# Kernel tuning notes

Hardware: AMD Instinct MI355X
Metric: run time of the kernel (lower is better)

## Reference

```python
import jax, jax.numpy as jnp
import numpy as np

B, C, H, W = 8, 256, 128, 128
CQ = C // 8


def setup_inputs() -> dict:
    key = jax.random.key(0)
    ks = jax.random.split(key, 8)
    s = 1.0 / np.sqrt(C)
    return {
        "x": jax.random.normal(ks[0], (B, C, H, W), dtype=jnp.float32),
        "wq": jax.random.normal(ks[1], (CQ, C), dtype=jnp.float32) * s,
        "bq": jax.random.normal(ks[2], (CQ,), dtype=jnp.float32) * 0.01,
        "wk": jax.random.normal(ks[3], (CQ, C), dtype=jnp.float32) * s,
        "bk": jax.random.normal(ks[4], (CQ,), dtype=jnp.float32) * 0.01,
        "wv": jax.random.normal(ks[5], (C, C), dtype=jnp.float32) * s,
        "bv": jax.random.normal(ks[6], (C,), dtype=jnp.float32) * 0.01,
        "gamma": jax.random.normal(ks[7], (1,), dtype=jnp.float32) * 0.1,
    }


def reference(x, wq, bq, wk, bk, wv, bv, gamma):
    b, c, h, w = x.shape
    # 1x1 convs == channel matmuls
    q = jnp.einsum("oc,bchw->bohw", wq, x) + bq[None, :, None, None]  # [B,Cq,H,W]
    k = jnp.einsum("oc,bchw->bohw", wk, x) + bk[None, :, None, None]  # [B,Cq,H,W]
    v = jnp.einsum("oc,bchw->bohw", wv, x) + bv[None, :, None, None]  # [B,C,H,W]

    # column (height) scores: energy_H[b,i,w,j] = <k[:, i, w], q[:, j, w]>, -inf on i==j
    e_h = jnp.einsum("bciw,bcjw->biwj", k, q)  # [B,H,W,H]
    diag = jnp.eye(h, dtype=bool)[:, None, :]  # [H,1,H] -> masks i==j
    e_h = jnp.where(diag[None], -jnp.inf, e_h)

    # row (width) scores: energy_W[b,h,i,j] = <k[:, h, i], q[:, h, j]>
    e_w = jnp.einsum("bchi,bchj->bhij", k, q)  # [B,H,W,W]

    # joint softmax over concatenated H+W scores (axis 3), as in the torch code
    att = jax.nn.softmax(jnp.concatenate([e_h, e_w], axis=3), axis=3)
    a_h, a_w = att[..., :h], att[..., h:]

    out_h = jnp.einsum("bciw,biwj->bcjw", v, a_h)  # aggregate along column
    out_w = jnp.einsum("bchi,bhij->bchj", v, a_w)  # aggregate along row
    return gamma * (out_h + out_w) + x
```

## Files before the change

### kernel.cpp

```cpp
#include <hip/hip_runtime.h>
#include <math.h>

#define C_   256
#define CQ_  32
#define H_   128
#define W_   128
#define HW_  (H_ * W_)
#define OC_  320

typedef __attribute__((ext_vector_type(8))) short  s8v;
typedef __attribute__((ext_vector_type(4))) float  f4v;
typedef __attribute__((ext_vector_type(8))) unsigned short u8v;
typedef __attribute__((ext_vector_type(4))) unsigned short u4v;

__device__ inline unsigned short f2bf(float f) {
    unsigned int u = __float_as_uint(f);
    unsigned int r = (u + 0x7fffu + ((u >> 16) & 1u)) >> 16;
    return (unsigned short)r;
}
__device__ inline float bfu(unsigned short u) {
    return __uint_as_float((unsigned int)u << 16);
}

__global__ __launch_bounds__(256) void k_wconv(
    const float* __restrict__ wq, const float* __restrict__ wk,
    const float* __restrict__ wv, unsigned short* __restrict__ Wb)
{
    int idx4 = blockIdx.x * 256 + threadIdx.x;
    int e = idx4 * 4;
    int oc = e >> 8, k = e & 255;
    const float* src;
    if (oc < 32)      src = wq + (size_t)oc * C_ + k;
    else if (oc < 64) src = wk + (size_t)(oc - 32) * C_ + k;
    else              src = wv + (size_t)(oc - 64) * C_ + k;
    float4 v = *(const float4*)src;
    u4v o;
    o[0] = f2bf(v.x); o[1] = f2bf(v.y); o[2] = f2bf(v.z); o[3] = f2bf(v.w);
    *(u4v*)(Wb + e) = o;
}

__global__ __launch_bounds__(256) void k_qkv(
    const float* __restrict__ x, const unsigned short* __restrict__ Wb,
    const float* __restrict__ bq, const float* __restrict__ bk,
    const float* __restrict__ bv,
    unsigned short* __restrict__ qkv, int b0)
{
    __shared__ __align__(16) unsigned short Wl[160][72];
    __shared__ __align__(16) unsigned int   Xp[32 * 132];
    const int t = threadIdx.x;
    const int lane = t & 63;
    const int wave = t >> 6;
    const int n0 = blockIdx.x * 128;
    const int ocblk = blockIdx.y * 160;
    const int bb = blockIdx.z;
    const float* xb = x + (size_t)(b0 + bb) * C_ * HW_;

    const int lg = lane >> 4;
    const int ll = lane & 15;
    const int n_w = wave * 32;

    const int kp8 = t >> 5;
    const int n4  = (t & 31) * 4;
    const int wrow = t >> 3;
    const int wcg  = (t & 7) * 8;
    float4 ra[4], rb[4];
    u8v wreg[5];

    #pragma unroll
    for (int p = 0; p < 4; ++p) {
        int krow = (p * 8 + kp8) * 2;
        ra[p] = *(const float4*)(xb + (size_t)krow * HW_ + n0 + n4);
        rb[p] = *(const float4*)(xb + (size_t)(krow + 1) * HW_ + n0 + n4);
    }
    #pragma unroll
    for (int q = 0; q < 5; ++q)
        wreg[q] = *(const u8v*)(Wb + (size_t)(ocblk + wrow + q * 32) * C_ + wcg);

    f4v acc[10][2];
    #pragma unroll
    for (int mr = 0; mr < 10; ++mr)
        #pragma unroll
        for (int nr = 0; nr < 2; ++nr)
            acc[mr][nr] = (f4v){0.f, 0.f, 0.f, 0.f};

    #pragma unroll
    for (int kc = 0; kc < 4; ++kc) {
        __syncthreads();
        #pragma unroll
        for (int p = 0; p < 4; ++p) {
            uint4 d;
            const float* af  = (const float*)&ra[p];
            const float* bf_ = (const float*)&rb[p];
            #pragma unroll
            for (int i = 0; i < 4; ++i) {
                unsigned int lo = (__float_as_uint(af[i])  + 0x8000u) >> 16;
                unsigned int hi = (__float_as_uint(bf_[i]) + 0x8000u) & 0xffff0000u;
                ((unsigned int*)&d)[i] = hi | lo;
            }
            *(uint4*)&Xp[(p * 8 + kp8) * 132 + n4] = d;
        }
        #pragma unroll
        for (int q = 0; q < 5; ++q)
            *(u8v*)&Wl[wrow + q * 32][wcg] = wreg[q];
        __syncthreads();
        if (kc < 3) {
            #pragma unroll
            for (int p = 0; p < 4; ++p) {
                int krow = (kc + 1) * 64 + (p * 8 + kp8) * 2;
                ra[p] = *(const float4*)(xb + (size_t)krow * HW_ + n0 + n4);
                rb[p] = *(const float4*)(xb + (size_t)(krow + 1) * HW_ + n0 + n4);
            }
            #pragma unroll
            for (int q = 0; q < 5; ++q)
                wreg[q] = *(const u8v*)(
                    Wb + (size_t)(ocblk + wrow + q * 32) * C_ + (kc + 1) * 64 + wcg);
        }
        #pragma unroll
        for (int ks = 0; ks < 2; ++ks) {
            s8v bfr[2];
            #pragma unroll
            for (int nr = 0; nr < 2; ++nr) {
                int4 bd;
                #pragma unroll
                for (int e2 = 0; e2 < 4; ++e2)
                    ((int*)&bd)[e2] =
                        Xp[(ks * 16 + lg * 4 + e2) * 132 + n_w + nr * 16 + ll];
                bfr[nr] = *(s8v*)&bd;
            }
            #pragma unroll
            for (int mr = 0; mr < 10; ++mr) {
                s8v afr = *(const s8v*)&Wl[mr * 16 + ll][ks * 32 + lg * 8];
                #pragma unroll
                for (int nr = 0; nr < 2; ++nr)
                    acc[mr][nr] = __builtin_amdgcn_mfma_f32_16x16x32_bf16(
                        afr, bfr[nr], acc[mr][nr], 0, 0, 0);
            }
        }
    }

    #pragma unroll
    for (int mr = 0; mr < 10; ++mr) {
        float bias[4];
        #pragma unroll
        for (int r = 0; r < 4; ++r) {
            int oc = ocblk + mr * 16 + lg * 4 + r;
            if (oc < 32)      bias[r] = bq[oc];
            else if (oc < 64) bias[r] = bk[oc - 32];
            else              bias[r] = bv[oc - 64];
        }
        #pragma unroll
        for (int nr = 0; nr < 2; ++nr) {
            int n = n0 + n_w + nr * 16 + ll;
            #pragma unroll
            for (int r = 0; r < 4; ++r) {
                int oc = ocblk + mr * 16 + lg * 4 + r;
                qkv[((size_t)bb * OC_ + oc) * HW_ + n] = f2bf(acc[mr][nr][r] + bias[r]);
            }
        }
    }
}

__global__ __launch_bounds__(256) void k_transpose_qkv(
    const unsigned short* __restrict__ qkv, unsigned short* __restrict__ qkv_t)
{
    __shared__ unsigned short tile[32][34];
    const int bb = blockIdx.z;
    const int oc = blockIdx.y;
    const int th = (blockIdx.x & 3) * 32;
    const int tw = (blockIdx.x >> 2) * 32;
    const unsigned short* src = qkv + ((size_t)bb * OC_ + oc) * HW_;
    #pragma unroll
    for (int r = 0; r < 4; ++r) {
        int h = threadIdx.y * 4 + r;
        tile[h][threadIdx.x] = src[(size_t)(th + h) * W_ + tw + threadIdx.x];
    }
    __syncthreads();
    unsigned short* dst = qkv_t + (size_t)bb * W_ * OC_ * H_;
    #pragma unroll
    for (int r = 0; r < 4; ++r) {
        int wl = threadIdx.y * 4 + r;
        dst[((size_t)(tw + wl) * OC_ + oc) * H_ + th + threadIdx.x] = tile[threadIdx.x][wl];
    }
}

__device__ inline void stage_KQ(const unsigned short* base, int cstride,
                                unsigned int* Ktp, unsigned int* Qp, int t)
{
    {
        int i = t & 127, half = t >> 7, c0 = half * 16;
        unsigned int kr[16];
        #pragma unroll
        for (int cc = 0; cc < 16; ++cc)
            kr[cc] = base[(size_t)(32 + c0 + cc) * cstride + i];
        uint4 d0, d1;
        #pragma unroll
        for (int e2 = 0; e2 < 4; ++e2)
            ((unsigned int*)&d0)[e2] = kr[2 * e2] | (kr[2 * e2 + 1] << 16);
        #pragma unroll
        for (int e2 = 0; e2 < 4; ++e2)
            ((unsigned int*)&d1)[e2] = kr[8 + 2 * e2] | (kr[9 + 2 * e2] << 16);
        *(uint4*)&Ktp[i * 20 + half * 8]     = d0;
        *(uint4*)&Ktp[i * 20 + half * 8 + 4] = d1;
    }
    {
        int c2 = t >> 4, j8 = (t & 15) * 8;
        u8v qa = *(const u8v*)(base + (size_t)(2 * c2) * cstride + j8);
        u8v qb = *(const u8v*)(base + (size_t)(2 * c2 + 1) * cstride + j8);
        uint4 e0, e1;
        #pragma unroll
        for (int e = 0; e < 4; ++e)
            ((unsigned int*)&e0)[e] =
                (unsigned int)qa[e] | ((unsigned int)qb[e] << 16);
        #pragma unroll
        for (int e = 0; e < 4; ++e)
            ((unsigned int*)&e1)[e] =
                (unsigned int)qa[4 + e] | ((unsigned int)qb[4 + e] << 16);
        *(uint4*)&Qp[c2 * 132 + j8]     = e0;
        *(uint4*)&Qp[c2 * 132 + j8 + 4] = e1;
    }
}

__device__ inline f4v eqk_mfma(const unsigned int* Ktp, const unsigned int* Qp,
                               int mr, int j, int lg, int ll)
{
    s8v afr = *(const s8v*)&Ktp[(mr * 16 + ll) * 20 + lg * 4];
    int4 bd;
    #pragma unroll
    for (int e2 = 0; e2 < 4; ++e2)
        ((int*)&bd)[e2] = Qp[(lg * 4 + e2) * 132 + j];
    s8v bfr = *(s8v*)&bd;
    return __builtin_amdgcn_mfma_f32_16x16x32_bf16(
        afr, bfr, (f4v){0.f, 0.f, 0.f, 0.f}, 0, 0, 0);
}

__global__ __launch_bounds__(256) void k_stats_h(
    const unsigned short* __restrict__ qkv_t,
    float* __restrict__ mh, float* __restrict__ sh)
{
    __shared__ __align__(16) unsigned int Ktp[128 * 20];
    __shared__ __align__(16) unsigned int Qp[16 * 132];
    const int t = threadIdx.x;
    const int beta = blockIdx.x;
    const int bb = blockIdx.y;
    const unsigned short* base = qkv_t + ((size_t)bb * W_ + beta) * OC_ * H_;
    stage_KQ(base, H_, Ktp, Qp, t);
    __syncthreads();

    const int lane = t & 63;
    const int wv = t >> 6;
    const int lg = lane >> 4;
    const int ll = lane & 15;

    #pragma unroll
    for (int ml = 0; ml < 2; ++ml) {
        const int mr = wv * 2 + ml;
        const int i0 = mr * 16 + lg * 4;
        f4v ef[8];
        #pragma unroll
        for (int nt = 0; nt < 8; ++nt) {
            f4v e = eqk_mfma(Ktp, Qp, mr, nt * 16 + ll, lg, ll);
            int j = nt * 16 + ll;
            #pragma unroll
            for (int r = 0; r < 4; ++r)
                if (i0 + r == j) e[r] = -INFINITY;
            ef[nt] = e;
        }
        #pragma unroll
        for (int r = 0; r < 4; ++r) {
            float mm = -INFINITY;
            #pragma unroll
            for (int nt = 0; nt < 8; ++nt) mm = fmaxf(mm, ef[nt][r]);
            #pragma unroll
            for (int s = 1; s < 16; s <<= 1) mm = fmaxf(mm, __shfl_xor(mm, s));
            float ss = 0.f;
            #pragma unroll
            for (int nt = 0; nt < 8; ++nt) ss += __expf(ef[nt][r] - mm);
            #pragma unroll
            for (int s = 1; s < 16; s <<= 1) ss += __shfl_xor(ss, s);
            if (ll == 0) {
                int i = i0 + r;
                mh[((size_t)bb * H_ + i) * W_ + beta] = mm;
                sh[((size_t)bb * H_ + i) * W_ + beta] = ss;
            }
        }
    }
}

__global__ __launch_bounds__(256) void k_stats_w(
    const unsigned short* __restrict__ qkv,
    float* __restrict__ mw, float* __restrict__ sw)
{
    __shared__ __align__(16) unsigned int Ktp[128 * 20];
    __shared__ __align__(16) unsigned int Qp[16 * 132];
    const int t = threadIdx.x;
    const int alpha = blockIdx.x;
    const int bb = blockIdx.y;
    const unsigned short* base = qkv + (size_t)bb * OC_ * HW_ + (size_t)alpha * W_;
    stage_KQ(base, HW_, Ktp, Qp, t);
    __syncthreads();

    const int lane = t & 63;
    const int wv = t >> 6;
    const int lg = lane >> 4;
    const int ll = lane & 15;

    #pragma unroll
    for (int ml = 0; ml < 2; ++ml) {
        const int mr = wv * 2 + ml;
        const int i0 = mr * 16 + lg * 4;
        f4v ef[8];
        #pragma unroll
        for (int nt = 0; nt < 8; ++nt)
            ef[nt] = eqk_mfma(Ktp, Qp, mr, nt * 16 + ll, lg, ll);
        #pragma unroll
        for (int r = 0; r < 4; ++r) {
            float mm = -INFINITY;
            #pragma unroll
            for (int nt = 0; nt < 8; ++nt) mm = fmaxf(mm, ef[nt][r]);
            #pragma unroll
            for (int s = 1; s < 16; s <<= 1) mm = fmaxf(mm, __shfl_xor(mm, s));
            float ss = 0.f;
            #pragma unroll
            for (int nt = 0; nt < 8; ++nt) ss += __expf(ef[nt][r] - mm);
            #pragma unroll
            for (int s = 1; s < 16; s <<= 1) ss += __shfl_xor(ss, s);
            if (ll == 0) {
                int i = i0 + r;
                mw[((size_t)bb * H_ + alpha) * W_ + i] = mm;
                sw[((size_t)bb * H_ + alpha) * W_ + i] = ss;
            }
        }
    }
}

__global__ __launch_bounds__(256) void k_prep(
    const float* __restrict__ mh, const float* __restrict__ sh,
    const float* __restrict__ mw, const float* __restrict__ sw,
    float* __restrict__ mc, float* __restrict__ dv,
    float* __restrict__ mct, float* __restrict__ dvt, int n)
{
    int idx = blockIdx.x * 256 + threadIdx.x;
    if (idx >= n) return;
    float m1 = mh[idx], s1 = sh[idx], m2 = mw[idx], s2 = sw[idx];
    float m = fmaxf(m1, m2);
    float d = 1.f / (s1 * __expf(m1 - m) + s2 * __expf(m2 - m));
    mc[idx] = m; dv[idx] = d;
    int q = idx & (W_ - 1);
    int p = (idx >> 7) & (H_ - 1);
    int b = idx >> 14;
    size_t tid = ((size_t)b * W_ + q) * H_ + p;
    mct[tid] = m; dvt[tid] = d;
}

__global__ __launch_bounds__(256) void k_outh(
    const unsigned short* __restrict__ qkv_t,
    const float* __restrict__ mct, const float* __restrict__ dvt,
    unsigned short* __restrict__ oh_t)
{
    __shared__ __align__(16) unsigned short Pt[128 * 128];
    __shared__ __align__(16) unsigned char  Ubuf[18688];
    __shared__ float mloc[128], dloc[128];
    unsigned int* Ktp = (unsigned int*)Ubuf;
    unsigned int* Qp  = (unsigned int*)(Ubuf + 10240);
    unsigned short* Vl = (unsigned short*)Ubuf;

    const int t = threadIdx.x;
    const int beta = blockIdx.x;
    const int bb = blockIdx.y;
    const unsigned short* base = qkv_t + ((size_t)bb * W_ + beta) * OC_ * H_;

    if (t < 128) {
        size_t sidx = ((size_t)bb * W_ + beta) * H_ + t;
        mloc[t] = mct[sidx];
        dloc[t] = dvt[sidx];
    }
    stage_KQ(base, H_, Ktp, Qp, t);

    const int vc  = t >> 4;
    const int vi0 = (t & 15) * 8;
    u8v vreg[4];
    {
        const unsigned short* vsrc = base + (size_t)64 * H_;
        #pragma unroll
        for (int q = 0; q < 4; ++q)
            vreg[q] = *(const u8v*)(vsrc + (size_t)(vc + q * 16) * H_ + vi0);
    }
    __syncthreads();

    const int lane = t & 63;
    const int wv = t >> 6;
    const int lg = lane >> 4;
    const int ll = lane & 15;
    const int jq0 = wv * 32;

    #pragma unroll
    for (int mr = 0; mr < 8; ++mr) {
        const int i0 = mr * 16 + lg * 4;
        float mi[4], di[4];
        #pragma unroll
        for (int r = 0; r < 4; ++r) { mi[r] = mloc[i0 + r]; di[r] = dloc[i0 + r]; }
        #pragma unroll
        for (int nt = 0; nt < 2; ++nt) {
            int j = jq0 + nt * 16 + ll;
            f4v e = eqk_mfma(Ktp, Qp, mr, j, lg, ll);
            float p0 = (i0     == j) ? 0.f : __expf(e[0] - mi[0]) * di[0];
            float p1 = (i0 + 1 == j) ? 0.f : __expf(e[1] - mi[1]) * di[1];
            float p2 = (i0 + 2 == j) ? 0.f : __expf(e[2] - mi[2]) * di[2];
            float p3 = (i0 + 3 == j) ? 0.f : __expf(e[3] - mi[3]) * di[3];
            uint2 wd;
            wd.x = f2bf(p0) | ((unsigned int)f2bf(p1) << 16);
            wd.y = f2bf(p2) | ((unsigned int)f2bf(p3) << 16);
            int sidx = (j * 128 + i0) ^ ((j & 7) << 3);
            *(uint2*)&Pt[sidx] = wd;
        }
    }

    unsigned short* outbase = oh_t + ((size_t)bb * W_ + beta) * C_ * H_;

    for (int ch = 0; ch < 4; ++ch) {
        __syncthreads();
        #pragma unroll
        for (int q = 0; q < 4; ++q) {
            int c = vc + q * 16;
            *(u8v*)&Vl[(c * 128 + vi0) ^ ((c & 7) << 3)] = vreg[q];
        }
        __syncthreads();
        if (ch < 3) {
            const unsigned short* vsrc = base + (size_t)(64 + (ch + 1) * 64) * H_;
            #pragma unroll
            for (int q = 0; q < 4; ++q)
                vreg[q] = *(const u8v*)(vsrc + (size_t)(vc + q * 16) * H_ + vi0);
        }

        f4v acc[8];
        #pragma unroll
        for (int nt = 0; nt < 8; ++nt) acc[nt] = (f4v){0.f, 0.f, 0.f, 0.f};

        #pragma unroll
        for (int kk = 0; kk < 4; ++kk) {
            int crow = wv * 16 + ll;
            s8v afr = *(const s8v*)&Vl[(crow * 128 + kk * 32 + lg * 8) ^ ((crow & 7) << 3)];
            #pragma unroll
            for (int nt = 0; nt < 8; ++nt) {
                int j = nt * 16 + ll;
                s8v bfr = *(const s8v*)&Pt[(j * 128 + kk * 32 + lg * 8) ^ ((j & 7) << 3)];
                acc[nt] = __builtin_amdgcn_mfma_f32_16x16x32_bf16(afr, bfr, acc[nt], 0, 0, 0);
            }
        }
        #pragma unroll
        for (int nt = 0; nt < 8; ++nt) {
            int j = nt * 16 + ll;
            #pragma unroll
            for (int r = 0; r < 4; ++r) {
                int c = ch * 64 + wv * 16 + lg * 4 + r;
                outbase[(size_t)c * H_ + j] = f2bf(acc[nt][r]);
            }
        }
    }
}

__global__ __launch_bounds__(256) void k_outw(
    const unsigned short* __restrict__ qkv,
    const float* __restrict__ mc, const float* __restrict__ dv_,
    unsigned short* __restrict__ ow)
{
    __shared__ __align__(16) unsigned short Pt[128 * 128];
    __shared__ __align__(16) unsigned char  Ubuf[18688];
    __shared__ float mloc[128], dloc[128];
    unsigned int* Ktp = (unsigned int*)Ubuf;
    unsigned int* Qp  = (unsigned int*)(Ubuf + 10240);
    unsigned short* Vl = (unsigned short*)Ubuf;

    const int t = threadIdx.x;
    const int alpha = blockIdx.x;
    const int bb = blockIdx.y;
    const unsigned short* base = qkv + (size_t)bb * OC_ * HW_ + (size_t)alpha * W_;

    if (t < 128) {
        size_t sidx = ((size_t)bb * H_ + alpha) * W_ + t;
        mloc[t] = mc[sidx];
        dloc[t] = dv_[sidx];
    }
    stage_KQ(base, HW_, Ktp, Qp, t);

    const int vc  = t >> 4;
    const int vi0 = (t & 15) * 8;
    u8v vreg[4];
    {
        const unsigned short* vsrc = base + (size_t)64 * HW_;
        #pragma unroll
        for (int q = 0; q < 4; ++q)
            vreg[q] = *(const u8v*)(vsrc + (size_t)(vc + q * 16) * HW_ + vi0);
    }
    __syncthreads();

    const int lane = t & 63;
    const int wv = t >> 6;
    const int lg = lane >> 4;
    const int ll = lane & 15;
    const int jq0 = wv * 32;

    #pragma unroll
    for (int mr = 0; mr < 8; ++mr) {
        const int i0 = mr * 16 + lg * 4;
        float mi[4], di[4];
        #pragma unroll
        for (int r = 0; r < 4; ++r) { mi[r] = mloc[i0 + r]; di[r] = dloc[i0 + r]; }
        #pragma unroll
        for (int nt = 0; nt < 2; ++nt) {
            int j = jq0 + nt * 16 + ll;
            f4v e = eqk_mfma(Ktp, Qp, mr, j, lg, ll);
            float p0 = __expf(e[0] - mi[0]) * di[0];
            float p1 = __expf(e[1] - mi[1]) * di[1];
            float p2 = __expf(e[2] - mi[2]) * di[2];
            float p3 = __expf(e[3] - mi[3]) * di[3];
            uint2 wd;
            wd.x = f2bf(p0) | ((unsigned int)f2bf(p1) << 16);
            wd.y = f2bf(p2) | ((unsigned int)f2bf(p3) << 16);
            int sidx = (j * 128 + i0) ^ ((j & 7) << 3);
            *(uint2*)&Pt[sidx] = wd;
        }
    }

    unsigned short* obase = ow + (size_t)bb * C_ * HW_ + (size_t)alpha * W_;

    for (int ch = 0; ch < 4; ++ch) {
        __syncthreads();
        #pragma unroll
        for (int q = 0; q < 4; ++q) {
            int c = vc + q * 16;
            *(u8v*)&Vl[(c * 128 + vi0) ^ ((c & 7) << 3)] = vreg[q];
        }
        __syncthreads();
        if (ch < 3) {
            const unsigned short* vsrc = base + (size_t)(64 + (ch + 1) * 64) * HW_;
            #pragma unroll
            for (int q = 0; q < 4; ++q)
                vreg[q] = *(const u8v*)(vsrc + (size_t)(vc + q * 16) * HW_ + vi0);
        }

        f4v acc[8];
        #pragma unroll
        for (int nt = 0; nt < 8; ++nt) acc[nt] = (f4v){0.f, 0.f, 0.f, 0.f};

        #pragma unroll
        for (int kk = 0; kk < 4; ++kk) {
            int crow = wv * 16 + ll;
            s8v afr = *(const s8v*)&Vl[(crow * 128 + kk * 32 + lg * 8) ^ ((crow & 7) << 3)];
            #pragma unroll
            for (int nt = 0; nt < 8; ++nt) {
                int j = nt * 16 + ll;
                s8v bfr = *(const s8v*)&Pt[(j * 128 + kk * 32 + lg * 8) ^ ((j & 7) << 3)];
                acc[nt] = __builtin_amdgcn_mfma_f32_16x16x32_bf16(afr, bfr, acc[nt], 0, 0, 0);
            }
        }
        #pragma unroll
        for (int nt = 0; nt < 8; ++nt) {
            int j = nt * 16 + ll;
            #pragma unroll
            for (int r = 0; r < 4; ++r) {
                int c = ch * 64 + wv * 16 + lg * 4 + r;
                obase[(size_t)c * HW_ + j] = f2bf(acc[nt][r]);
            }
        }
    }
}

__global__ __launch_bounds__(256) void k_combine(
    const unsigned short* __restrict__ oh_t, const unsigned short* __restrict__ ow,
    const float* __restrict__ x, const float* __restrict__ gamma_p,
    float* __restrict__ out, int b0)
{
    __shared__ float tile[32][33];
    const int bb = blockIdx.z;
    const int c = blockIdx.y;
    const int th = (blockIdx.x & 3) * 32;
    const int tw = (blockIdx.x >> 2) * 32;
    const float gamma = gamma_p[0];
    const unsigned short* src = oh_t + (size_t)bb * W_ * C_ * H_;
    #pragma unroll
    for (int r = 0; r < 4; ++r) {
        int wl = threadIdx.y * 4 + r;
        tile[wl][threadIdx.x] =
            bfu(src[((size_t)(tw + wl) * C_ + c) * H_ + th + threadIdx.x]);
    }
    __syncthreads();
    const size_t pbase = ((size_t)bb * C_ + c) * HW_;
    const size_t gbase = ((size_t)(b0 + bb) * C_ + c) * HW_;
    #pragma unroll
    for (int r = 0; r < 4; ++r) {
        int hl = threadIdx.y * 4 + r;
        size_t idx = (size_t)(th + hl) * W_ + tw + threadIdx.x;
        float owv = bfu(ow[pbase + idx]);
        out[gbase + idx] = x[gbase + idx] + gamma * (owv + tile[threadIdx.x][hl]);
    }
}

extern "C" void kernel_launch(void* const* d_in, const int* in_sizes, int n_in,
                              void* d_out, int out_size, void* d_ws, size_t ws_size,
                              hipStream_t stream)
{
    (void)in_sizes; (void)n_in; (void)out_size;
    const float* x  = (const float*)d_in[0];
    const float* wq = (const float*)d_in[1];
    const float* bq = (const float*)d_in[2];
    const float* wk = (const float*)d_in[3];
    const float* bk = (const float*)d_in[4];
    const float* wv = (const float*)d_in[5];
    const float* bv = (const float*)d_in[6];
    const float* gm = (const float*)d_in[7];
    float* out = (float*)d_out;

    const size_t e_qkv  = (size_t)OC_ * HW_;
    const size_t e_out  = (size_t)C_ * HW_;
    const size_t e_stat = (size_t)HW_;
    const size_t perb_bytes = (e_qkv * 2 + e_out * 2) * 2 + e_stat * 8 * 4;
    const size_t wb_bytes = (size_t)OC_ * C_ * 2;
    int nbcap = (int)((ws_size - wb_bytes) / perb_bytes);
    if (nbcap > 8) nbcap = 8;
    if (nbcap < 1) nbcap = 1;

    unsigned short* Wb    = (unsigned short*)d_ws;
    unsigned short* qkv   = Wb    + (size_t)OC_ * C_;
    unsigned short* qkv_t = qkv   + e_qkv * nbcap;
    unsigned short* oh    = qkv_t + e_qkv * nbcap;
    unsigned short* ow    = oh    + e_out * nbcap;
    float* mh  = (float*)(ow + e_out * nbcap);
    float* sh  = mh  + e_stat * nbcap;
    float* mw  = sh  + e_stat * nbcap;
    float* sw  = mw  + e_stat * nbcap;
    float* mc  = sw  + e_stat * nbcap;
    float* dv  = mc  + e_stat * nbcap;
    float* mct = dv  + e_stat * nbcap;
    float* dvt = mct + e_stat * nbcap;

    k_wconv<<<dim3(80), 256, 0, stream>>>(wq, wk, wv, Wb);

    for (int b0 = 0; b0 < 8; b0 += nbcap) {
        int nb = 8 - b0 < nbcap ? 8 - b0 : nbcap;
        k_qkv<<<dim3(HW_ / 128, 2, nb), 256, 0, stream>>>(
            x, Wb, bq, bk, bv, qkv, b0);
        k_transpose_qkv<<<dim3(16, OC_, nb), dim3(32, 8), 0, stream>>>(qkv, qkv_t);
        k_stats_h<<<dim3(W_, nb), 256, 0, stream>>>(qkv_t, mh, sh);
        k_stats_w<<<dim3(H_, nb), 256, 0, stream>>>(qkv, mw, sw);
        int nstat = nb * HW_;
        k_prep<<<dim3((nstat + 255) / 256), 256, 0, stream>>>(
            mh, sh, mw, sw, mc, dv, mct, dvt, nstat);
        k_outh<<<dim3(W_, nb), 256, 0, stream>>>(qkv_t, mct, dvt, oh);
        k_outw<<<dim3(H_, nb), 256, 0, stream>>>(qkv, mc, dv, ow);
        k_combine<<<dim3(16, C_, nb), dim3(32, 8), 0, stream>>>(
            oh, ow, x, gm, out, b0);
    }
}
```

Measured before the change: 304.8 us.

## Shrink QKV tile with double-buffered LDS and retile PV waves to 32x64

The QKV projection kernel now computes 64 output channels per block instead of 160, which raises the grid from 2 to 5 blocks in y. It double-buffers the LDS tiles so one barrier per K chunk is needed and global loads run two chunks ahead. In the outh/outw kernels each wave now computes a 32-channel by 64-position tile instead of 16 by 128, so V and P fragments are reused across more MFMAs and fewer LDS reads are issued. In exchange, x is re-read from global memory by more blocks, and the staging uses more LDS.

```diff
diff --git a/kernel.cpp b/kernel.cpp
--- a/kernel.cpp
+++ b/kernel.cpp
@@ -45,13 +45,13 @@
     const float* __restrict__ bv,
     unsigned short* __restrict__ qkv, int b0)
 {
-    __shared__ __align__(16) unsigned short Wl[160][72];
-    __shared__ __align__(16) unsigned int   Xp[32 * 132];
+    __shared__ __align__(16) unsigned short Wl[2][64][72];
+    __shared__ __align__(16) unsigned int   Xp[2][32 * 132];
     const int t = threadIdx.x;
     const int lane = t & 63;
     const int wave = t >> 6;
     const int n0 = blockIdx.x * 128;
-    const int ocblk = blockIdx.y * 160;
+    const int ocblk = blockIdx.y * 64;
     const int bb = blockIdx.z;
     const float* xb = x + (size_t)(b0 + bb) * C_ * HW_;
 
@@ -64,7 +64,7 @@
     const int wrow = t >> 3;
     const int wcg  = (t & 7) * 8;
     float4 ra[4], rb[4];
-    u8v wreg[5];
+    u8v wreg[2];
 
     #pragma unroll
     for (int p = 0; p < 4; ++p) {
@@ -73,73 +73,103 @@
         rb[p] = *(const float4*)(xb + (size_t)(krow + 1) * HW_ + n0 + n4);
     }
     #pragma unroll
-    for (int q = 0; q < 5; ++q)
+    for (int q = 0; q < 2; ++q)
         wreg[q] = *(const u8v*)(Wb + (size_t)(ocblk + wrow + q * 32) * C_ + wcg);
 
-    f4v acc[10][2];
-    #pragma unroll
-    for (int mr = 0; mr < 10; ++mr)
+    #pragma unroll
+    for (int p = 0; p < 4; ++p) {
+        uint4 d;
+        const float* af  = (const float*)&ra[p];
+        const float* bf_ = (const float*)&rb[p];
+        #pragma unroll
+        for (int i = 0; i < 4; ++i) {
+            unsigned int lo = (__float_as_uint(af[i])  + 0x8000u) >> 16;
+            unsigned int hi = (__float_as_uint(bf_[i]) + 0x8000u) & 0xffff0000u;
+            ((unsigned int*)&d)[i] = hi | lo;
+        }
+        *(uint4*)&Xp[0][(p * 8 + kp8) * 132 + n4] = d;
+    }
+    #pragma unroll
+    for (int q = 0; q < 2; ++q)
+        *(u8v*)&Wl[0][wrow + q * 32][wcg] = wreg[q];
+
+    #pragma unroll
+    for (int p = 0; p < 4; ++p) {
+        int krow = 64 + (p * 8 + kp8) * 2;
+        ra[p] = *(const float4*)(xb + (size_t)krow * HW_ + n0 + n4);
+        rb[p] = *(const float4*)(xb + (size_t)(krow + 1) * HW_ + n0 + n4);
+    }
+    #pragma unroll
+    for (int q = 0; q < 2; ++q)
+        wreg[q] = *(const u8v*)(Wb + (size_t)(ocblk + wrow + q * 32) * C_ + 64 + wcg);
+
+    f4v acc[4][2];
+    #pragma unroll
+    for (int mr = 0; mr < 4; ++mr)
         #pragma unroll
         for (int nr = 0; nr < 2; ++nr)
             acc[mr][nr] = (f4v){0.f, 0.f, 0.f, 0.f};
 
+    __syncthreads();
+
     #pragma unroll
     for (int kc = 0; kc < 4; ++kc) {
-        __syncthreads();
-        #pragma unroll
-        for (int p = 0; p < 4; ++p) {
-            uint4 d;
-            const float* af  = (const float*)&ra[p];
-            const float* bf_ = (const float*)&rb[p];
-            #pragma unroll
-            for (int i = 0; i < 4; ++i) {
-                unsigned int lo = (__float_as_uint(af[i])  + 0x8000u) >> 16;
-                unsigned int hi = (__float_as_uint(bf_[i]) + 0x8000u) & 0xffff0000u;
-                ((unsigned int*)&d)[i] = hi | lo;
-            }
-            *(uint4*)&Xp[(p * 8 + kp8) * 132 + n4] = d;
-        }
-        #pragma unroll
-        for (int q = 0; q < 5; ++q)
-            *(u8v*)&Wl[wrow + q * 32][wcg] = wreg[q];
-        __syncthreads();
+        const int cur = kc & 1;
         if (kc < 3) {
             #pragma unroll
             for (int p = 0; p < 4; ++p) {
-                int krow = (kc + 1) * 64 + (p * 8 + kp8) * 2;
+                uint4 d;
+                const float* af  = (const float*)&ra[p];
+                const float* bf_ = (const float*)&rb[p];
+                #pragma unroll
+                for (int i = 0; i < 4; ++i) {
+                    unsigned int lo = (__float_as_uint(af[i])  + 0x8000u) >> 16;
+                    unsigned int hi = (__float_as_uint(bf_[i]) + 0x8000u) & 0xffff0000u;
+                    ((unsigned int*)&d)[i] = hi | lo;
+                }
+                *(uint4*)&Xp[cur ^ 1][(p * 8 + kp8) * 132 + n4] = d;
+            }
+            #pragma unroll
+            for (int q = 0; q < 2; ++q)
+                *(u8v*)&Wl[cur ^ 1][wrow + q * 32][wcg] = wreg[q];
+        }
+        if (kc < 2) {
+            #pragma unroll
+            for (int p = 0; p < 4; ++p) {
+                int krow = (kc + 2) * 64 + (p * 8 + kp8) * 2;
                 ra[p] = *(const float4*)(xb + (size_t)krow * HW_ + n0 + n4);
                 rb[p] = *(const float4*)(xb + (size_t)(krow + 1) * HW_ + n0 + n4);
             }
             #pragma unroll
-            for (int q = 0; q < 5; ++q)
+            for (int q = 0; q < 2; ++q)
                 wreg[q] = *(const u8v*)(
-                    Wb + (size_t)(ocblk + wrow + q * 32) * C_ + (kc + 1) * 64 + wcg);
+                    Wb + (size_t)(ocblk + wrow + q * 32) * C_ + (kc + 2) * 64 + wcg);
         }
         #pragma unroll
         for (int ks = 0; ks < 2; ++ks) {
-            s8v bfr[2];
+            s8v afr[4];
+            #pragma unroll
+            for (int mr = 0; mr < 4; ++mr)
+                afr[mr] = *(const s8v*)&Wl[cur][mr * 16 + ll][ks * 32 + lg * 8];
             #pragma unroll
             for (int nr = 0; nr < 2; ++nr) {
                 int4 bd;
                 #pragma unroll
                 for (int e2 = 0; e2 < 4; ++e2)
                     ((int*)&bd)[e2] =
-                        Xp[(ks * 16 + lg * 4 + e2) * 132 + n_w + nr * 16 + ll];
-                bfr[nr] = *(s8v*)&bd;
-            }
-            #pragma unroll
-            for (int mr = 0; mr < 10; ++mr) {
-                s8v afr = *(const s8v*)&Wl[mr * 16 + ll][ks * 32 + lg * 8];
+                        Xp[cur][(ks * 16 + lg * 4 + e2) * 132 + n_w + nr * 16 + ll];
+                s8v bfr = *(s8v*)&bd;
                 #pragma unroll
-                for (int nr = 0; nr < 2; ++nr)
+                for (int mr = 0; mr < 4; ++mr)
                     acc[mr][nr] = __builtin_amdgcn_mfma_f32_16x16x32_bf16(
-                        afr, bfr[nr], acc[mr][nr], 0, 0, 0);
-            }
-        }
-    }
-
-    #pragma unroll
-    for (int mr = 0; mr < 10; ++mr) {
+                        afr[mr], bfr, acc[mr][nr], 0, 0, 0);
+            }
+        }
+        __syncthreads();
+    }
+
+    #pragma unroll
+    for (int mr = 0; mr < 4; ++mr) {
         float bias[4];
         #pragma unroll
         for (int r = 0; r < 4; ++r) {
@@ -416,6 +446,8 @@
     }
 
     unsigned short* outbase = oh_t + ((size_t)bb * W_ + beta) * C_ * H_;
+    const int cw = (wv & 1) * 32;
+    const int jw = (wv >> 1) * 64;
 
     for (int ch = 0; ch < 4; ++ch) {
         __syncthreads();
@@ -432,30 +464,40 @@
                 vreg[q] = *(const u8v*)(vsrc + (size_t)(vc + q * 16) * H_ + vi0);
         }
 
-        f4v acc[8];
-        #pragma unroll
-        for (int nt = 0; nt < 8; ++nt) acc[nt] = (f4v){0.f, 0.f, 0.f, 0.f};
+        f4v acc[2][4];
+        #pragma unroll
+        for (int cr = 0; cr < 2; ++cr)
+            #pragma unroll
+            for (int nt = 0; nt < 4; ++nt)
+                acc[cr][nt] = (f4v){0.f, 0.f, 0.f, 0.f};
 
         #pragma unroll
         for (int kk = 0; kk < 4; ++kk) {
-            int crow = wv * 16 + ll;
-            s8v afr = *(const s8v*)&Vl[(crow * 128 + kk * 32 + lg * 8) ^ ((crow & 7) << 3)];
-            #pragma unroll
-            for (int nt = 0; nt < 8; ++nt) {
-                int j = nt * 16 + ll;
+            s8v afr[2];
+            #pragma unroll
+            for (int cr = 0; cr < 2; ++cr) {
+                int crow = cw + cr * 16 + ll;
+                afr[cr] = *(const s8v*)&Vl[(crow * 128 + kk * 32 + lg * 8) ^ ((crow & 7) << 3)];
+            }
+            #pragma unroll
+            for (int nt = 0; nt < 4; ++nt) {
+                int j = jw + nt * 16 + ll;
                 s8v bfr = *(const s8v*)&Pt[(j * 128 + kk * 32 + lg * 8) ^ ((j & 7) << 3)];
-                acc[nt] = __builtin_amdgcn_mfma_f32_16x16x32_bf16(afr, bfr, acc[nt], 0, 0, 0);
-            }
-        }
-        #pragma unroll
-        for (int nt = 0; nt < 8; ++nt) {
-            int j = nt * 16 + ll;
-            #pragma unroll
-            for (int r = 0; r < 4; ++r) {
-                int c = ch * 64 + wv * 16 + lg * 4 + r;
-                outbase[(size_t)c * H_ + j] = f2bf(acc[nt][r]);
-            }
-        }
+                acc[0][nt] = __builtin_amdgcn_mfma_f32_16x16x32_bf16(afr[0], bfr, acc[0][nt], 0, 0, 0);
+                acc[1][nt] = __builtin_amdgcn_mfma_f32_16x16x32_bf16(afr[1], bfr, acc[1][nt], 0, 0, 0);
+            }
+        }
+        #pragma unroll
+        for (int cr = 0; cr < 2; ++cr)
+            #pragma unroll
+            for (int nt = 0; nt < 4; ++nt) {
+                int j = jw + nt * 16 + ll;
+                #pragma unroll
+                for (int r = 0; r < 4; ++r) {
+                    int c = ch * 64 + cw + cr * 16 + lg * 4 + r;
+                    outbase[(size_t)c * H_ + j] = f2bf(acc[cr][nt][r]);
+                }
+            }
     }
 }
 
@@ -523,6 +565,8 @@
     }
 
     unsigned short* obase = ow + (size_t)bb * C_ * HW_ + (size_t)alpha * W_;
+    const int cw = (wv & 1) * 32;
+    const int jw = (wv >> 1) * 64;
 
     for (int ch = 0; ch < 4; ++ch) {
         __syncthreads();
@@ -539,30 +583,40 @@
                 vreg[q] = *(const u8v*)(vsrc + (size_t)(vc + q * 16) * HW_ + vi0);
         }
 
-        f4v acc[8];
-        #pragma unroll
-        for (int nt = 0; nt < 8; ++nt) acc[nt] = (f4v){0.f, 0.f, 0.f, 0.f};
+        f4v acc[2][4];
+        #pragma unroll
+        for (int cr = 0; cr < 2; ++cr)
+            #pragma unroll
+            for (int nt = 0; nt < 4; ++nt)
+                acc[cr][nt] = (f4v){0.f, 0.f, 0.f, 0.f};
 
         #pragma unroll
         for (int kk = 0; kk < 4; ++kk) {
-            int crow = wv * 16 + ll;
-            s8v afr = *(const s8v*)&Vl[(crow * 128 + kk * 32 + lg * 8) ^ ((crow & 7) << 3)];
-            #pragma unroll
-            for (int nt = 0; nt < 8; ++nt) {
-                int j = nt * 16 + ll;
+            s8v afr[2];
+            #pragma unroll
+            for (int cr = 0; cr < 2; ++cr) {
+                int crow = cw + cr * 16 + ll;
+                afr[cr] = *(const s8v*)&Vl[(crow * 128 + kk * 32 + lg * 8) ^ ((crow & 7) << 3)];
+            }
+            #pragma unroll
+            for (int nt = 0; nt < 4; ++nt) {
+                int j = jw + nt * 16 + ll;
                 s8v bfr = *(const s8v*)&Pt[(j * 128 + kk * 32 + lg * 8) ^ ((j & 7) << 3)];
-                acc[nt] = __builtin_amdgcn_mfma_f32_16x16x32_bf16(afr, bfr, acc[nt], 0, 0, 0);
-            }
-        }
-        #pragma unroll
-        for (int nt = 0; nt < 8; ++nt) {
-            int j = nt * 16 + ll;
-            #pragma unroll
-            for (int r = 0; r < 4; ++r) {
-                int c = ch * 64 + wv * 16 + lg * 4 + r;
-                obase[(size_t)c * HW_ + j] = f2bf(acc[nt][r]);
-            }
-        }
+                acc[0][nt] = __builtin_amdgcn_mfma_f32_16x16x32_bf16(afr[0], bfr, acc[0][nt], 0, 0, 0);
+                acc[1][nt] = __builtin_amdgcn_mfma_f32_16x16x32_bf16(afr[1], bfr, acc[1][nt], 0, 0, 0);
+            }
+        }
+        #pragma unroll
+        for (int cr = 0; cr < 2; ++cr)
+            #pragma unroll
+            for (int nt = 0; nt < 4; ++nt) {
+                int j = jw + nt * 16 + ll;
+                #pragma unroll
+                for (int r = 0; r < 4; ++r) {
+                    int c = ch * 64 + cw + cr * 16 + lg * 4 + r;
+                    obase[(size_t)c * HW_ + j] = f2bf(acc[cr][nt][r]);
+                }
+            }
     }
 }
 
@@ -638,7 +692,7 @@
 
     for (int b0 = 0; b0 < 8; b0 += nbcap) {
         int nb = 8 - b0 < nbcap ? 8 - b0 : nbcap;
-        k_qkv<<<dim3(HW_ / 128, 2, nb), 256, 0, stream>>>(
+        k_qkv<<<dim3(HW_ / 128, 5, nb), 256, 0, stream>>>(
             x, Wb, bq, bk, bv, qkv, b0);
         k_transpose_qkv<<<dim3(16, OC_, nb), dim3(32, 8), 0, stream>>>(qkv, qkv_t);
         k_stats_h<<<dim3(W_, nb), 256, 0, stream>>>(qkv_t, mh, sh);
```

Measured after the change: 289.9 us. -4.9%, faster.
